# Optimization experiments

Hardware: AMD Instinct MI355X
Metric: run time of the kernel (lower is better)

Reference implementation:

```python
import jax, jax.numpy as jnp
import numpy as np

EPS = 1e-5        # LayerNorm eps (torch default)
BETA = 1.0e12     # Hopfield scaling -> near-hard nearest-pattern retrieval


def _ln(x, g, b):
    mu = jnp.mean(x, axis=-1, keepdims=True)
    var = jnp.var(x, axis=-1, keepdims=True)
    return (x - mu) * jax.lax.rsqrt(var + EPS) * g + b


def setup_inputs() -> dict:
    key = jax.random.key(0)
    ks = jax.random.split(key, 10)
    B, S, D_IN, Q, P, D_OUT, N_CLS = 32768, 16, 14, 256, 256, 28, 7

    def n(k, shape, scale=1.0):
        return jax.random.normal(k, shape, dtype=jnp.float32) * scale

    return {
        "x": n(ks[0], (B, S, D_IN)),                 # (batch, bands=16, 14)
        "lookup": n(ks[1], (1, Q, D_IN)),            # learned stored patterns
        "g_st": jnp.ones((D_IN,), jnp.float32),      # LN stored pattern
        "b_st": jnp.zeros((D_IN,), jnp.float32),
        "g_sp": jnp.ones((D_IN,), jnp.float32),      # LN state pattern
        "b_sp": jnp.zeros((D_IN,), jnp.float32),
        "g_pp": jnp.ones((D_IN,), jnp.float32),      # LN pattern projection
        "b_pp": jnp.zeros((D_IN,), jnp.float32),
        "Wv": n(ks[2], (P, D_IN), 1.0 / np.sqrt(D_IN)),   # value proj 14->256 (no bias)
        "Wo": n(ks[3], (D_OUT, P), 1.0 / np.sqrt(P)),     # out proj 256->28 (no bias)
        "Wm": n(ks[4], (N_CLS, D_OUT), 1.0 / np.sqrt(D_OUT)),  # Linear_m 28->7
        "bm": n(ks[5], (N_CLS,), 0.1),
        "Wb": n(ks[6], (1, S), 1.0 / np.sqrt(S)),          # Linear_b 16->1
        "bb": n(ks[7], (1,), 0.1),
    }


def reference(x, lookup, g_st, b_st, g_sp, b_sp, g_pp, b_pp,
              Wv, Wo, Wm, bm, Wb, bb):
    # --- HopfieldLayer (num_heads=1, static Q/K, projected V) ---
    q = _ln(x, g_sp, b_sp)                       # state pattern, (B,S,14)
    k = _ln(lookup[0], g_st, b_st)               # stored patterns, (Q,14)
    v = _ln(lookup[0], g_pp, b_pp) @ Wv.T        # (Q,256)
    logits = BETA * jnp.einsum('bsd,qd->bsq', q, k)   # (B,S,Q)
    attn = jax.nn.softmax(logits, axis=-1)       # near one-hot retrieval
    h = jnp.einsum('bsq,qp->bsp', attn, v)       # (B,S,256)
    hop = h @ Wo.T                                # (B,S,28)
    # --- head ---
    y = hop @ Wm.T + bm                           # (B,S,7)
    y = jnp.swapaxes(y, 1, 2)                     # (B,7,S) == einsum 'abc->acb'
    z = y @ Wb.T + bb                             # (B,7,1)
    return jax.nn.softmax(z[:, :, 0], axis=1)     # (B,7)
```

## Files before the change

### kernel.cpp

```cpp
#include <hip/hip_runtime.h>
#include <math.h>

#define BATCH 32768
#define SS 16
#define DI 14
#define BQ 256
#define NC 7
#define NBLK 2048

#define WS_MPACK_OFF 0
#define WS_TF_OFF    28672
#define WS_ZB_OFF    35840
#define WS_CV_OFF    35896
#define WS_HC_OFF    37944

typedef float  f32x4 __attribute__((ext_vector_type(4)));
typedef short  s16x8 __attribute__((ext_vector_type(8)));
typedef float  v2f   __attribute__((ext_vector_type(2)));

__device__ __forceinline__ unsigned short bf16_rne(float f) {
    unsigned u = __float_as_uint(f);
    unsigned r = u + 0x7FFFu + ((u >> 16) & 1u);
    return (unsigned short)(r >> 16);
}
__device__ __forceinline__ float bf16_to_f32(unsigned short h) {
    return __uint_as_float(((unsigned)h) << 16);
}

__device__ __forceinline__ double pack_key(float v, int j) {
    unsigned u = __float_as_uint(v);
    u ^= ((unsigned)((int)u >> 31)) | 0x80000000u;
    const unsigned long long k =
        ((unsigned long long)u << 8) | (unsigned long long)(255 - j);
    return __longlong_as_double((long long)k);
}

__global__ __launch_bounds__(256) void precompute_kernel(
    const float* __restrict__ lookup,
    const float* __restrict__ g_st, const float* __restrict__ b_st,
    const float* __restrict__ g_pp, const float* __restrict__ b_pp,
    const float* __restrict__ g_sp, const float* __restrict__ b_sp,
    const float* __restrict__ Wv,  const float* __restrict__ Wo,
    const float* __restrict__ Wm,  const float* __restrict__ bm,
    const float* __restrict__ Wb,  const float* __restrict__ bb,
    double2* __restrict__ mpack, float* __restrict__ Tf, double* __restrict__ zb,
    double* __restrict__ cvec, int* __restrict__ hc)
{
    __shared__ double G1s[256][7];
    __shared__ double Gs[14][7];
    const int tid = threadIdx.x;

    {
        const int p = tid;
        for (int c = 0; c < NC; ++c) {
            double acc = 0.0;
            for (int o = 0; o < 28; ++o)
                acc += (double)Wo[o * 256 + p] * (double)Wm[c * 28 + o];
            G1s[p][c] = acc;
        }
    }
    __syncthreads();
    if (tid < DI * NC) {
        const int d = tid / NC, c = tid % NC;
        double acc = 0.0;
        for (int p = 0; p < 256; ++p)
            acc += (double)Wv[p * DI + d] * G1s[p][c];
        Gs[d][c] = acc;
    }
    __syncthreads();

    {
        const int j = tid;
        double xr[DI];
        double sum = 0.0;
        for (int d = 0; d < DI; ++d) { xr[d] = (double)lookup[j * DI + d]; sum += xr[d]; }
        const double mu = sum * (1.0 / (double)DI);
        double vs = 0.0;
        for (int d = 0; d < DI; ++d) { const double t = xr[d] - mu; vs += t * t; }
        const double rs = 1.0 / sqrt(vs * (1.0 / (double)DI) + 1e-5);

        double kj[DI], vl[DI];
        for (int d = 0; d < DI; ++d) {
            const double nrm = (xr[d] - mu) * rs;
            kj[d] = nrm * (double)g_st[d] + (double)b_st[d];
            vl[d] = nrm * (double)g_pp[d] + (double)b_pp[d];
        }
        double mv[DI], S = 0.0, cj = 0.0;
        for (int d = 0; d < DI; ++d) {
            mv[d] = kj[d] * (double)g_sp[d];
            S += mv[d];
            cj += (double)b_sp[d] * kj[d];
        }
        const double Sm = S * (1.0 / (double)DI);
        for (int d2 = 0; d2 < DI / 2; ++d2) {
            double2 p; p.x = mv[2 * d2] - Sm; p.y = mv[2 * d2 + 1] - Sm;
            mpack[d2 * 256 + j] = p;
        }
        cvec[j] = cj;

        for (int c = 0; c < NC; ++c) {
            double acc = 0.0;
            for (int d = 0; d < DI; ++d) acc += vl[d] * Gs[d][c];
            Tf[j * NC + c] = (float)acc;
        }
    }
    if (tid < NC) {
        double wbsum = 0.0;
        for (int s = 0; s < SS; ++s) wbsum += (double)Wb[s];
        zb[tid] = (double)bm[tid] * wbsum + (double)bb[0];
    }
    if (tid == 0) {
        int f = 0;
        for (int d = 0; d < DI; ++d) f |= (b_sp[d] != 0.0f) ? 1 : 0;
        *hc = f;
    }
}

__global__ __launch_bounds__(256, 4) void hopfield_kernel(
    const float* __restrict__ x,
    const double2* __restrict__ mpack, const double* __restrict__ cvec,
    const int* __restrict__ hcp,
    const float* __restrict__ Tf, const double* __restrict__ zb,
    const float* __restrict__ Wb, float* __restrict__ out)
{
    __shared__ s16x8  bhiS[16 * 32];
    __shared__ s16x8  bloS[16 * 32];
    __shared__ float  Ts[256 * NC];
    __shared__ double zbs[NC];
    __shared__ float  wbs[SS];
    __shared__ int    jcandS[4][4][SS][2];
    __shared__ int    jstarS[4][4][SS];
    __shared__ double zrowd[4][4][NC];
    __shared__ float  irsS[4][4][SS];

    const int tid  = threadIdx.x;
    const int lane = tid & 63;
    const int w    = tid >> 6;
    const int g    = lane >> 4;
    const int l    = lane & 15;
    const int hc   = *hcp;

    {
        const int j = tid;
        float mf[16];
        #pragma unroll
        for (int d2 = 0; d2 < 7; ++d2) {
            const double2 mv = mpack[d2 * 256 + j];
            mf[2 * d2] = (float)mv.x; mf[2 * d2 + 1] = (float)mv.y;
        }
        mf[14] = (float)cvec[j];
        mf[15] = 0.f;
        #pragma unroll
        for (int ks = 0; ks < 2; ++ks) {
            s16x8 h8, l8;
            #pragma unroll
            for (int i = 0; i < 8; ++i) {
                const float f = mf[8 * ks + i];
                const unsigned short h = bf16_rne(f);
                const float r = f - bf16_to_f32(h);
                h8[i] = (short)h;
                l8[i] = (short)bf16_rne(r);
            }
            bhiS[(j >> 4) * 32 + ks * 16 + (j & 15)] = h8;
            bloS[(j >> 4) * 32 + ks * 16 + (j & 15)] = l8;
        }
    }
    for (int i = tid; i < 256 * NC; i += 256) Ts[i] = Tf[i];
    if (tid < NC) zbs[tid] = zb[tid];
    if (tid < SS) wbs[tid] = Wb[tid];
    __syncthreads();

    const int gw = blockIdx.x * 4 + w;
    const float* xw = x + (size_t)gw * 4 * SS * DI;

    if (hc) {
        const int bi = lane >> 4, s = lane & 15;
        const float* xr = xw + (bi * SS + s) * DI;
        float xv[DI]; float sum = 0.f;
        #pragma unroll
        for (int d = 0; d < DI; ++d) { xv[d] = xr[d]; sum += xv[d]; }
        const float mu = sum * (1.0f / (float)DI);
        float vs = 0.f;
        #pragma unroll
        for (int d = 0; d < DI; ++d) { const float t = xv[d] - mu; vs += t * t; }
        irsS[w][bi][s] = 1.0f / sqrtf(vs * (1.0f / (float)DI) + 1e-5f);
        __builtin_amdgcn_wave_barrier();
    }

    for (int bi = 0; bi < 4; ++bi) {
        s16x8 ah = {0,0,0,0,0,0,0,0}, al = {0,0,0,0,0,0,0,0};
        if (lane < 32) {
            const float* xr = xw + (bi * SS + l) * DI;
            float xv[8];
            if (g == 0) {
                #pragma unroll
                for (int i = 0; i < 4; ++i) {
                    const v2f p = *(const v2f*)(xr + 2 * i);
                    xv[2 * i] = p.x; xv[2 * i + 1] = p.y;
                }
            } else {
                #pragma unroll
                for (int i = 0; i < 3; ++i) {
                    const v2f p = *(const v2f*)(xr + 8 + 2 * i);
                    xv[2 * i] = p.x; xv[2 * i + 1] = p.y;
                }
                xv[6] = hc ? irsS[w][bi][l] : 0.f;
                xv[7] = 0.f;
            }
            #pragma unroll
            for (int i = 0; i < 8; ++i) {
                const unsigned short h = bf16_rne(xv[i]);
                const float r = xv[i] - bf16_to_f32(h);
                ah[i] = (short)h;
                al[i] = (short)bf16_rne(r);
            }
        }

        float t0v[4], t1v[4]; int t0j[4], t1j[4];
        #pragma unroll
        for (int r = 0; r < 4; ++r) {
            t0v[r] = -INFINITY; t1v[r] = -INFINITY; t0j[r] = 0; t1j[r] = 1;
        }
        const f32x4 z4 = {0.f, 0.f, 0.f, 0.f};

        #pragma unroll
        for (int t = 0; t < 16; ++t) {
            s16x8 bh = {0,0,0,0,0,0,0,0}, bl = {0,0,0,0,0,0,0,0};
            if (lane < 32) { bh = bhiS[t * 32 + lane]; bl = bloS[t * 32 + lane]; }
            f32x4 acc = __builtin_amdgcn_mfma_f32_16x16x32_bf16(al, bh, z4, 0, 0, 0);
            acc = __builtin_amdgcn_mfma_f32_16x16x32_bf16(ah, bl, acc, 0, 0, 0);
            acc = __builtin_amdgcn_mfma_f32_16x16x32_bf16(ah, bh, acc, 0, 0, 0);
            #pragma unroll
            for (int r = 0; r < 4; ++r) {
                const float s = acc[r];
                if (t & 1) {
                    const bool c = s > t1v[r];
                    t1v[r] = c ? s : t1v[r]; t1j[r] = c ? t : t1j[r];
                } else {
                    const bool c = s > t0v[r];
                    t0v[r] = c ? s : t0v[r]; t0j[r] = c ? t : t0j[r];
                }
            }
        }

        double kh[4], kl[4];
        #pragma unroll
        for (int r = 0; r < 4; ++r) {
            const double k0 = pack_key(t0v[r], t0j[r] * 16 + l);
            const double k1 = pack_key(t1v[r], t1j[r] * 16 + l);
            kh[r] = fmax(k0, k1);
            kl[r] = fmin(k0, k1);
        }
        #pragma unroll
        for (int off = 8; off > 0; off >>= 1) {
            #pragma unroll
            for (int r = 0; r < 4; ++r) {
                const double oh = __shfl_down(kh[r], (unsigned)off, 16);
                const double ol = __shfl_down(kl[r], (unsigned)off, 16);
                const double nh = fmax(kh[r], oh);
                const double nl = fmax(fmin(kh[r], oh), fmax(kl[r], ol));
                kh[r] = nh; kl[r] = nl;
            }
        }
        if (l == 0) {
            #pragma unroll
            for (int r = 0; r < 4; ++r) {
                jcandS[w][bi][g * 4 + r][0] = 255 - (int)(__double_as_longlong(kh[r]) & 0xFF);
                jcandS[w][bi][g * 4 + r][1] = 255 - (int)(__double_as_longlong(kl[r]) & 0xFF);
            }
        }
    }
    __builtin_amdgcn_wave_barrier();

    #pragma unroll
    for (int u = 0; u < 2; ++u) {
        const int task = u * 64 + lane;
        const int bi = task >> 5, row = (task >> 1) & 15, ci = task & 1;
        const int j = jcandS[w][bi][row][ci];
        const float* xr = xw + (bi * SS + row) * DI;
        double a = 0.0;
        #pragma unroll
        for (int d2 = 0; d2 < 7; ++d2) {
            const v2f xp = *(const v2f*)(xr + 2 * d2);
            const double2 mv = mpack[d2 * 256 + j];
            a += (double)xp.x * mv.x + (double)xp.y * mv.y;
        }
        if (hc) {
            double xv[DI]; double sum = 0.0;
            #pragma unroll
            for (int d = 0; d < DI; ++d) { xv[d] = (double)xr[d]; sum += xv[d]; }
            const double mu = sum * (1.0 / (double)DI);
            double vs = 0.0;
            #pragma unroll
            for (int d = 0; d < DI; ++d) { const double t = xv[d] - mu; vs += t * t; }
            const double irs64 = 1.0 / sqrt(vs * (1.0 / (double)DI) + 1e-5);
            a += irs64 * cvec[j];
        }
        const double oa = __shfl_xor(a, 1);
        const int    oj = __shfl_xor(j, 1);
        const int jwin = (a > oa || (a == oa && j < oj)) ? j : oj;
        if ((lane & 1) == 0) jstarS[w][bi][row] = jwin;
    }
    __builtin_amdgcn_wave_barrier();

    if (lane < 4 * NC) {
        const int bi = lane / NC, c = lane % NC;
        double zv = zbs[c];
        #pragma unroll
        for (int s = 0; s < SS; ++s)
            zv += (double)wbs[s] * (double)Ts[jstarS[w][bi][s] * NC + c];
        zrowd[w][bi][c] = zv;
    }
    __builtin_amdgcn_wave_barrier();
    if (lane < 4 * NC) {
        const int bi = lane / NC;
        double m = zrowd[w][bi][0];
        #pragma unroll
        for (int c2 = 1; c2 < NC; ++c2) m = fmax(m, zrowd[w][bi][c2]);
        float den = 0.f;
        #pragma unroll
        for (int c2 = 0; c2 < NC; ++c2) den += __expf((float)(zrowd[w][bi][c2] - m));
        const float num = __expf((float)(zrowd[w][bi][lane % NC] - m));
        out[(size_t)gw * 28 + lane] = num / den;
    }
}

extern "C" void kernel_launch(void* const* d_in, const int* in_sizes, int n_in,
                              void* d_out, int out_size, void* d_ws, size_t ws_size,
                              hipStream_t stream) {
    const float* x      = (const float*)d_in[0];
    const float* lookup = (const float*)d_in[1];
    const float* g_st   = (const float*)d_in[2];
    const float* b_st   = (const float*)d_in[3];
    const float* g_sp   = (const float*)d_in[4];
    const float* b_sp   = (const float*)d_in[5];
    const float* g_pp   = (const float*)d_in[6];
    const float* b_pp   = (const float*)d_in[7];
    const float* Wv     = (const float*)d_in[8];
    const float* Wo     = (const float*)d_in[9];
    const float* Wm     = (const float*)d_in[10];
    const float* bm     = (const float*)d_in[11];
    const float* Wb     = (const float*)d_in[12];
    const float* bb     = (const float*)d_in[13];

    double2* mpack = (double2*)((char*)d_ws + WS_MPACK_OFF);
    float*   Tf    = (float*)((char*)d_ws + WS_TF_OFF);
    double*  zbp   = (double*)((char*)d_ws + WS_ZB_OFF);
    double*  cvec  = (double*)((char*)d_ws + WS_CV_OFF);
    int*     hc    = (int*)((char*)d_ws + WS_HC_OFF);

    precompute_kernel<<<1, 256, 0, stream>>>(lookup, g_st, b_st, g_pp, b_pp,
                                             g_sp, b_sp,
                                             Wv, Wo, Wm, bm, Wb, bb,
                                             mpack, Tf, zbp, cvec, hc);
    hopfield_kernel<<<NBLK, 256, 0, stream>>>(x, mpack, cvec, hc, Tf, zbp, Wb,
                                              (float*)d_out);
}
```

Before: 161.7 us.

## Halve batches per wave, double grid, interleave MFMA, use 32-bit swizzle top-2 reduction

```diff
diff --git a/kernel.cpp b/kernel.cpp
--- a/kernel.cpp
+++ b/kernel.cpp
@@ -6,7 +6,7 @@
 #define DI 14
 #define BQ 256
 #define NC 7
-#define NBLK 2048
+#define NBLK 4096
 
 #define WS_MPACK_OFF 0
 #define WS_TF_OFF    28672
@@ -27,12 +27,15 @@
     return __uint_as_float(((unsigned)h) << 16);
 }
 
-__device__ __forceinline__ double pack_key(float v, int j) {
+__device__ __forceinline__ unsigned key32(float v, int j) {
     unsigned u = __float_as_uint(v);
     u ^= ((unsigned)((int)u >> 31)) | 0x80000000u;
-    const unsigned long long k =
-        ((unsigned long long)u << 8) | (unsigned long long)(255 - j);
-    return __longlong_as_double((long long)k);
+    return (u & 0xFFFFFF00u) | (unsigned)(255 - j);
+}
+
+template<int PAT>
+__device__ __forceinline__ unsigned swz(unsigned v) {
+    return (unsigned)__builtin_amdgcn_ds_swizzle((int)v, PAT);
 }
 
 __global__ __launch_bounds__(256) void precompute_kernel(
@@ -123,15 +126,15 @@
     const float* __restrict__ Tf, const double* __restrict__ zb,
     const float* __restrict__ Wb, float* __restrict__ out)
 {
-    __shared__ s16x8  bhiS[16 * 32];
-    __shared__ s16x8  bloS[16 * 32];
+    __shared__ s16x8  bhiS[512];
+    __shared__ s16x8  bloS[512];
     __shared__ float  Ts[256 * NC];
     __shared__ double zbs[NC];
     __shared__ float  wbs[SS];
-    __shared__ int    jcandS[4][4][SS][2];
-    __shared__ int    jstarS[4][4][SS];
-    __shared__ double zrowd[4][4][NC];
-    __shared__ float  irsS[4][4][SS];
+    __shared__ int    jcandS[4][2][SS][2];
+    __shared__ int    jstarS[4][2][SS];
+    __shared__ double zrowd[4][2][NC];
+    __shared__ float  irsS[4][2][SS];
 
     const int tid  = threadIdx.x;
     const int lane = tid & 63;
@@ -171,25 +174,29 @@
     __syncthreads();
 
     const int gw = blockIdx.x * 4 + w;
-    const float* xw = x + (size_t)gw * 4 * SS * DI;
+    const float* xw = x + (size_t)gw * 2 * SS * DI;
 
     if (hc) {
-        const int bi = lane >> 4, s = lane & 15;
-        const float* xr = xw + (bi * SS + s) * DI;
-        float xv[DI]; float sum = 0.f;
-        #pragma unroll
-        for (int d = 0; d < DI; ++d) { xv[d] = xr[d]; sum += xv[d]; }
-        const float mu = sum * (1.0f / (float)DI);
-        float vs = 0.f;
-        #pragma unroll
-        for (int d = 0; d < DI; ++d) { const float t = xv[d] - mu; vs += t * t; }
-        irsS[w][bi][s] = 1.0f / sqrtf(vs * (1.0f / (float)DI) + 1e-5f);
+        if (lane < 32) {
+            const int bi = lane >> 4, s = lane & 15;
+            const float* xr = xw + (bi * SS + s) * DI;
+            float xv[DI]; float sum = 0.f;
+            #pragma unroll
+            for (int d = 0; d < DI; ++d) { xv[d] = xr[d]; sum += xv[d]; }
+            const float mu = sum * (1.0f / (float)DI);
+            float vs = 0.f;
+            #pragma unroll
+            for (int d = 0; d < DI; ++d) { const float t = xv[d] - mu; vs += t * t; }
+            irsS[w][bi][s] = 1.0f / sqrtf(vs * (1.0f / (float)DI) + 1e-5f);
+        }
         __builtin_amdgcn_wave_barrier();
     }
 
-    for (int bi = 0; bi < 4; ++bi) {
-        s16x8 ah = {0,0,0,0,0,0,0,0}, al = {0,0,0,0,0,0,0,0};
-        if (lane < 32) {
+    s16x8 ah[2] = {{0,0,0,0,0,0,0,0}, {0,0,0,0,0,0,0,0}};
+    s16x8 al[2] = {{0,0,0,0,0,0,0,0}, {0,0,0,0,0,0,0,0}};
+    if (lane < 32) {
+        #pragma unroll
+        for (int bi = 0; bi < 2; ++bi) {
             const float* xr = xw + (bi * SS + l) * DI;
             float xv[8];
             if (g == 0) {
@@ -211,71 +218,98 @@
             for (int i = 0; i < 8; ++i) {
                 const unsigned short h = bf16_rne(xv[i]);
                 const float r = xv[i] - bf16_to_f32(h);
-                ah[i] = (short)h;
-                al[i] = (short)bf16_rne(r);
-            }
-        }
-
-        float t0v[4], t1v[4]; int t0j[4], t1j[4];
+                ah[bi][i] = (short)h;
+                al[bi][i] = (short)bf16_rne(r);
+            }
+        }
+    }
+
+    float t0v[2][4], t1v[2][4]; int t0j[2][4], t1j[2][4];
+    #pragma unroll
+    for (int bi = 0; bi < 2; ++bi)
         #pragma unroll
         for (int r = 0; r < 4; ++r) {
-            t0v[r] = -INFINITY; t1v[r] = -INFINITY; t0j[r] = 0; t1j[r] = 1;
-        }
-        const f32x4 z4 = {0.f, 0.f, 0.f, 0.f};
-
-        #pragma unroll
-        for (int t = 0; t < 16; ++t) {
-            s16x8 bh = {0,0,0,0,0,0,0,0}, bl = {0,0,0,0,0,0,0,0};
-            if (lane < 32) { bh = bhiS[t * 32 + lane]; bl = bloS[t * 32 + lane]; }
-            f32x4 acc = __builtin_amdgcn_mfma_f32_16x16x32_bf16(al, bh, z4, 0, 0, 0);
-            acc = __builtin_amdgcn_mfma_f32_16x16x32_bf16(ah, bl, acc, 0, 0, 0);
-            acc = __builtin_amdgcn_mfma_f32_16x16x32_bf16(ah, bh, acc, 0, 0, 0);
+            t0v[bi][r] = -INFINITY; t1v[bi][r] = -INFINITY;
+            t0j[bi][r] = 0;         t1j[bi][r] = 1;
+        }
+    const f32x4 z4 = {0.f, 0.f, 0.f, 0.f};
+
+    #pragma unroll
+    for (int t = 0; t < 16; ++t) {
+        s16x8 bh = {0,0,0,0,0,0,0,0}, bl = {0,0,0,0,0,0,0,0};
+        if (lane < 32) { bh = bhiS[t * 32 + lane]; bl = bloS[t * 32 + lane]; }
+        #pragma unroll
+        for (int bi = 0; bi < 2; ++bi) {
+            f32x4 acc = __builtin_amdgcn_mfma_f32_16x16x32_bf16(al[bi], bh, z4, 0, 0, 0);
+            acc = __builtin_amdgcn_mfma_f32_16x16x32_bf16(ah[bi], bl, acc, 0, 0, 0);
+            acc = __builtin_amdgcn_mfma_f32_16x16x32_bf16(ah[bi], bh, acc, 0, 0, 0);
             #pragma unroll
             for (int r = 0; r < 4; ++r) {
                 const float s = acc[r];
                 if (t & 1) {
-                    const bool c = s > t1v[r];
-                    t1v[r] = c ? s : t1v[r]; t1j[r] = c ? t : t1j[r];
+                    const bool c = s > t1v[bi][r];
+                    t1v[bi][r] = c ? s : t1v[bi][r]; t1j[bi][r] = c ? t : t1j[bi][r];
                 } else {
-                    const bool c = s > t0v[r];
-                    t0v[r] = c ? s : t0v[r]; t0j[r] = c ? t : t0j[r];
+                    const bool c = s > t0v[bi][r];
+                    t0v[bi][r] = c ? s : t0v[bi][r]; t0j[bi][r] = c ? t : t0j[bi][r];
                 }
             }
         }
-
-        double kh[4], kl[4];
+    }
+
+    #pragma unroll
+    for (int bi = 0; bi < 2; ++bi) {
+        unsigned kh[4], kl[4];
         #pragma unroll
         for (int r = 0; r < 4; ++r) {
-            const double k0 = pack_key(t0v[r], t0j[r] * 16 + l);
-            const double k1 = pack_key(t1v[r], t1j[r] * 16 + l);
-            kh[r] = fmax(k0, k1);
-            kl[r] = fmin(k0, k1);
-        }
-        #pragma unroll
-        for (int off = 8; off > 0; off >>= 1) {
+            const unsigned k0 = key32(t0v[bi][r], t0j[bi][r] * 16 + l);
+            const unsigned k1 = key32(t1v[bi][r], t1j[bi][r] * 16 + l);
+            kh[r] = k0 > k1 ? k0 : k1;
+            kl[r] = k0 > k1 ? k1 : k0;
+        }
+        #pragma unroll
+        for (int r = 0; r < 4; ++r) {
+            {
+                const unsigned oh = swz<0x201F>(kh[r]), ol = swz<0x201F>(kl[r]);
+                const unsigned mn = kh[r] < oh ? kh[r] : oh;
+                kh[r] = kh[r] > oh ? kh[r] : oh;
+                const unsigned mx = kl[r] > ol ? kl[r] : ol;
+                kl[r] = mn > mx ? mn : mx;
+            }
+            {
+                const unsigned oh = swz<0x101F>(kh[r]), ol = swz<0x101F>(kl[r]);
+                const unsigned mn = kh[r] < oh ? kh[r] : oh;
+                kh[r] = kh[r] > oh ? kh[r] : oh;
+                const unsigned mx = kl[r] > ol ? kl[r] : ol;
+                kl[r] = mn > mx ? mn : mx;
+            }
+            {
+                const unsigned oh = swz<0x081F>(kh[r]), ol = swz<0x081F>(kl[r]);
+                const unsigned mn = kh[r] < oh ? kh[r] : oh;
+                kh[r] = kh[r] > oh ? kh[r] : oh;
+                const unsigned mx = kl[r] > ol ? kl[r] : ol;
+                kl[r] = mn > mx ? mn : mx;
+            }
+            {
+                const unsigned oh = swz<0x041F>(kh[r]), ol = swz<0x041F>(kl[r]);
+                const unsigned mn = kh[r] < oh ? kh[r] : oh;
+                kh[r] = kh[r] > oh ? kh[r] : oh;
+                const unsigned mx = kl[r] > ol ? kl[r] : ol;
+                kl[r] = mn > mx ? mn : mx;
+            }
+        }
+        if (l == 0) {
             #pragma unroll
             for (int r = 0; r < 4; ++r) {
-                const double oh = __shfl_down(kh[r], (unsigned)off, 16);
-                const double ol = __shfl_down(kl[r], (unsigned)off, 16);
-                const double nh = fmax(kh[r], oh);
-                const double nl = fmax(fmin(kh[r], oh), fmax(kl[r], ol));
-                kh[r] = nh; kl[r] = nl;
-            }
-        }
-        if (l == 0) {
-            #pragma unroll
-            for (int r = 0; r < 4; ++r) {
-                jcandS[w][bi][g * 4 + r][0] = 255 - (int)(__double_as_longlong(kh[r]) & 0xFF);
-                jcandS[w][bi][g * 4 + r][1] = 255 - (int)(__double_as_longlong(kl[r]) & 0xFF);
+                jcandS[w][bi][g * 4 + r][0] = 255 - (int)(kh[r] & 0xFFu);
+                jcandS[w][bi][g * 4 + r][1] = 255 - (int)(kl[r] & 0xFFu);
             }
         }
     }
     __builtin_amdgcn_wave_barrier();
 
-    #pragma unroll
-    for (int u = 0; u < 2; ++u) {
-        const int task = u * 64 + lane;
-        const int bi = task >> 5, row = (task >> 1) & 15, ci = task & 1;
+    {
+        const int bi = lane >> 5, row = (lane >> 1) & 15, ci = lane & 1;
         const int j = jcandS[w][bi][row][ci];
         const float* xr = xw + (bi * SS + row) * DI;
         double a = 0.0;
@@ -299,12 +333,13 @@
         const double oa = __shfl_xor(a, 1);
         const int    oj = __shfl_xor(j, 1);
         const int jwin = (a > oa || (a == oa && j < oj)) ? j : oj;
-        if ((lane & 1) == 0) jstarS[w][bi][row] = jwin;
+        if (ci == 0) jstarS[w][bi][row] = jwin;
     }
     __builtin_amdgcn_wave_barrier();
 
-    if (lane < 4 * NC) {
-        const int bi = lane / NC, c = lane % NC;
+    if (lane < 2 * NC) {
+        const int bi = lane >= NC ? 1 : 0;
+        const int c  = lane - bi * NC;
         double zv = zbs[c];
         #pragma unroll
         for (int s = 0; s < SS; ++s)
@@ -312,16 +347,17 @@
         zrowd[w][bi][c] = zv;
     }
     __builtin_amdgcn_wave_barrier();
-    if (lane < 4 * NC) {
-        const int bi = lane / NC;
+    if (lane < 2 * NC) {
+        const int bi = lane >= NC ? 1 : 0;
+        const int c  = lane - bi * NC;
         double m = zrowd[w][bi][0];
         #pragma unroll
         for (int c2 = 1; c2 < NC; ++c2) m = fmax(m, zrowd[w][bi][c2]);
         float den = 0.f;
         #pragma unroll
         for (int c2 = 0; c2 < NC; ++c2) den += __expf((float)(zrowd[w][bi][c2] - m));
-        const float num = __expf((float)(zrowd[w][bi][lane % NC] - m));
-        out[(size_t)gw * 28 + lane] = num / den;
+        const float num = __expf((float)(zrowd[w][bi][c] - m));
+        out[(size_t)gw * 2 * NC + lane] = num / den;
     }
 }
 
```

Result: slower. 185.4 us (+14.7%).

## Transpose MFMA operands so top-2 reduction uses in-lane merges and 32-bit keys

Applied to the files above, without the earlier changes.

```diff
diff --git a/kernel.cpp b/kernel.cpp
--- a/kernel.cpp
+++ b/kernel.cpp
@@ -27,12 +27,15 @@
     return __uint_as_float(((unsigned)h) << 16);
 }
 
-__device__ __forceinline__ double pack_key(float v, int j) {
+__device__ __forceinline__ unsigned key32(float v, int j) {
     unsigned u = __float_as_uint(v);
     u ^= ((unsigned)((int)u >> 31)) | 0x80000000u;
-    const unsigned long long k =
-        ((unsigned long long)u << 8) | (unsigned long long)(255 - j);
-    return __longlong_as_double((long long)k);
+    return (u & 0xFFFFFF00u) | (unsigned)(255 - j);
+}
+
+template<int PAT>
+__device__ __forceinline__ unsigned swz(unsigned v) {
+    return (unsigned)__builtin_amdgcn_ds_swizzle((int)v, PAT);
 }
 
 __global__ __launch_bounds__(256) void precompute_kernel(
@@ -125,7 +128,6 @@
 {
     __shared__ s16x8  bhiS[16 * 32];
     __shared__ s16x8  bloS[16 * 32];
-    __shared__ float  Ts[256 * NC];
     __shared__ double zbs[NC];
     __shared__ float  wbs[SS];
     __shared__ int    jcandS[4][4][SS][2];
@@ -165,7 +167,6 @@
             bloS[(j >> 4) * 32 + ks * 16 + (j & 15)] = l8;
         }
     }
-    for (int i = tid; i < 256 * NC; i += 256) Ts[i] = Tf[i];
     if (tid < NC) zbs[tid] = zb[tid];
     if (tid < SS) wbs[tid] = Wb[tid];
     __syncthreads();
@@ -188,7 +189,7 @@
     }
 
     for (int bi = 0; bi < 4; ++bi) {
-        s16x8 ah = {0,0,0,0,0,0,0,0}, al = {0,0,0,0,0,0,0,0};
+        s16x8 xh = {0,0,0,0,0,0,0,0}, xl = {0,0,0,0,0,0,0,0};
         if (lane < 32) {
             const float* xr = xw + (bi * SS + l) * DI;
             float xv[8];
@@ -211,63 +212,80 @@
             for (int i = 0; i < 8; ++i) {
                 const unsigned short h = bf16_rne(xv[i]);
                 const float r = xv[i] - bf16_to_f32(h);
-                ah[i] = (short)h;
-                al[i] = (short)bf16_rne(r);
+                xh[i] = (short)h;
+                xl[i] = (short)bf16_rne(r);
             }
         }
 
-        float t0v[4], t1v[4]; int t0j[4], t1j[4];
+        float tv[4][2]; int ti[4][2];
         #pragma unroll
         for (int r = 0; r < 4; ++r) {
-            t0v[r] = -INFINITY; t1v[r] = -INFINITY; t0j[r] = 0; t1j[r] = 1;
+            tv[r][0] = -INFINITY; tv[r][1] = -INFINITY;
+            ti[r][0] = 0;         ti[r][1] = 1;
         }
         const f32x4 z4 = {0.f, 0.f, 0.f, 0.f};
 
         #pragma unroll
         for (int t = 0; t < 16; ++t) {
-            s16x8 bh = {0,0,0,0,0,0,0,0}, bl = {0,0,0,0,0,0,0,0};
-            if (lane < 32) { bh = bhiS[t * 32 + lane]; bl = bloS[t * 32 + lane]; }
-            f32x4 acc = __builtin_amdgcn_mfma_f32_16x16x32_bf16(al, bh, z4, 0, 0, 0);
-            acc = __builtin_amdgcn_mfma_f32_16x16x32_bf16(ah, bl, acc, 0, 0, 0);
-            acc = __builtin_amdgcn_mfma_f32_16x16x32_bf16(ah, bh, acc, 0, 0, 0);
+            s16x8 ph = {0,0,0,0,0,0,0,0}, pl = {0,0,0,0,0,0,0,0};
+            if (lane < 32) { ph = bhiS[t * 32 + lane]; pl = bloS[t * 32 + lane]; }
+            f32x4 acc = __builtin_amdgcn_mfma_f32_16x16x32_bf16(pl, xh, z4, 0, 0, 0);
+            acc = __builtin_amdgcn_mfma_f32_16x16x32_bf16(ph, xl, acc, 0, 0, 0);
+            acc = __builtin_amdgcn_mfma_f32_16x16x32_bf16(ph, xh, acc, 0, 0, 0);
             #pragma unroll
             for (int r = 0; r < 4; ++r) {
                 const float s = acc[r];
                 if (t & 1) {
-                    const bool c = s > t1v[r];
-                    t1v[r] = c ? s : t1v[r]; t1j[r] = c ? t : t1j[r];
+                    const bool c = s > tv[r][1];
+                    tv[r][1] = c ? s : tv[r][1]; ti[r][1] = c ? t : ti[r][1];
                 } else {
-                    const bool c = s > t0v[r];
-                    t0v[r] = c ? s : t0v[r]; t0j[r] = c ? t : t0j[r];
+                    const bool c = s > tv[r][0];
+                    tv[r][0] = c ? s : tv[r][0]; ti[r][0] = c ? t : ti[r][0];
                 }
             }
         }
 
-        double kh[4], kl[4];
+        const int jbase = (lane & 0x30) >> 2;
+        unsigned h4[4], l4[4];
         #pragma unroll
         for (int r = 0; r < 4; ++r) {
-            const double k0 = pack_key(t0v[r], t0j[r] * 16 + l);
-            const double k1 = pack_key(t1v[r], t1j[r] * 16 + l);
-            kh[r] = fmax(k0, k1);
-            kl[r] = fmin(k0, k1);
-        }
-        #pragma unroll
-        for (int off = 8; off > 0; off >>= 1) {
-            #pragma unroll
-            for (int r = 0; r < 4; ++r) {
-                const double oh = __shfl_down(kh[r], (unsigned)off, 16);
-                const double ol = __shfl_down(kl[r], (unsigned)off, 16);
-                const double nh = fmax(kh[r], oh);
-                const double nl = fmax(fmin(kh[r], oh), fmax(kl[r], ol));
-                kh[r] = nh; kl[r] = nl;
-            }
-        }
-        if (l == 0) {
-            #pragma unroll
-            for (int r = 0; r < 4; ++r) {
-                jcandS[w][bi][g * 4 + r][0] = 255 - (int)(__double_as_longlong(kh[r]) & 0xFF);
-                jcandS[w][bi][g * 4 + r][1] = 255 - (int)(__double_as_longlong(kl[r]) & 0xFF);
-            }
+            const unsigned k0 = key32(tv[r][0], ti[r][0] * 16 + jbase + r);
+            const unsigned k1 = key32(tv[r][1], ti[r][1] * 16 + jbase + r);
+            h4[r] = k0 > k1 ? k0 : k1;
+            l4[r] = k0 > k1 ? k1 : k0;
+        }
+        unsigned H0, L0, H1, L1, kh, kl;
+        {   const unsigned mn = h4[0] < h4[1] ? h4[0] : h4[1];
+            H0 = h4[0] > h4[1] ? h4[0] : h4[1];
+            const unsigned mx = l4[0] > l4[1] ? l4[0] : l4[1];
+            L0 = mn > mx ? mn : mx; }
+        {   const unsigned mn = h4[2] < h4[3] ? h4[2] : h4[3];
+            H1 = h4[2] > h4[3] ? h4[2] : h4[3];
+            const unsigned mx = l4[2] > l4[3] ? l4[2] : l4[3];
+            L1 = mn > mx ? mn : mx; }
+        {   const unsigned mn = H0 < H1 ? H0 : H1;
+            kh = H0 > H1 ? H0 : H1;
+            const unsigned mx = L0 > L1 ? L0 : L1;
+            kl = mn > mx ? mn : mx; }
+
+        {
+            const unsigned oh = swz<0x401F>(kh), ol = swz<0x401F>(kl);
+            const unsigned mn = kh < oh ? kh : oh;
+            kh = kh > oh ? kh : oh;
+            const unsigned mx = kl > ol ? kl : ol;
+            kl = mn > mx ? mn : mx;
+        }
+        {
+            const unsigned oh = (unsigned)__shfl_xor((int)kh, 32);
+            const unsigned ol = (unsigned)__shfl_xor((int)kl, 32);
+            const unsigned mn = kh < oh ? kh : oh;
+            kh = kh > oh ? kh : oh;
+            const unsigned mx = kl > ol ? kl : ol;
+            kl = mn > mx ? mn : mx;
+        }
+        if (lane < 16) {
+            jcandS[w][bi][lane][0] = 255 - (int)(kh & 0xFFu);
+            jcandS[w][bi][lane][1] = 255 - (int)(kl & 0xFFu);
         }
     }
     __builtin_amdgcn_wave_barrier();
@@ -308,7 +326,7 @@
         double zv = zbs[c];
         #pragma unroll
         for (int s = 0; s < SS; ++s)
-            zv += (double)wbs[s] * (double)Ts[jstarS[w][bi][s] * NC + c];
+            zv += (double)wbs[s] * (double)Tf[jstarS[w][bi][s] * NC + c];
         zrowd[w][bi][c] = zv;
     }
     __builtin_amdgcn_wave_barrier();
```

New measurement: 150.4 us. -7.0%, faster.
